# Performance work log

Measured on AMD Instinct MI355X. Metric: run time of the kernel, lower is better.

Reference implementation:

```python
import jax, jax.numpy as jnp
import numpy as np

# Module config (matches init_kwargs shape_data=[8,32,32], pow=1, spde_type='adv_diff')
N_T, N_Y, N_X = 8, 32, 32
N = N_Y * N_X            # nb_nodes
DX = DY = DT = 1.0


def build_A(kappa, m1, m2, h11, h12, h22):
    """Dense [N,N] advection-diffusion operator A = kappa^2 I + m.grad - div(H grad),
    central differences on the n_y x n_x grid, zero-Dirichlet boundary (9-pt stencil).
    All coefficient inputs are [N] vectors (node-wise)."""
    ii, jj = jnp.divmod(jnp.arange(N), N_X)   # ii: y index, jj: x index
    rows = jnp.arange(N)
    A = jnp.zeros((N, N), dtype=kappa.dtype)
    # center
    A = A.at[rows, rows].add(kappa ** 2 + 2.0 * h11 / DX**2 + 2.0 * h22 / DY**2)

    def add(A, di, dj, coef):
        vi, vj = ii + di, jj + dj
        valid = (vi >= 0) & (vi < N_Y) & (vj >= 0) & (vj < N_X)
        cols = jnp.clip(vi, 0, N_Y - 1) * N_X + jnp.clip(vj, 0, N_X - 1)
        return A.at[rows, cols].add(jnp.where(valid, coef, 0.0))

    A = add(A, 0, +1, -h11 / DX**2 + m1 / (2.0 * DX))
    A = add(A, 0, -1, -h11 / DX**2 - m1 / (2.0 * DX))
    A = add(A, +1, 0, -h22 / DY**2 + m2 / (2.0 * DY))
    A = add(A, -1, 0, -h22 / DY**2 - m2 / (2.0 * DY))
    cxy = h12 / (2.0 * DX * DY)    # cross term -2*H12*u_xy with /(4 dx dy) stencil
    A = add(A, +1, +1, -cxy)
    A = add(A, -1, -1, -cxy)
    A = add(A, +1, -1, +cxy)
    A = add(A, -1, +1, +cxy)
    return A


def _forward(kappa, m, H, tau):
    n_b = kappa.shape[0]
    # reorder field params to [n_b, n_t, N]
    kap = jnp.moveaxis(kappa[:, 0], -1, 1)
    m1 = jnp.moveaxis(m[:, 0], -1, 1)
    m2 = jnp.moveaxis(m[:, 1], -1, 1)
    h11 = jnp.moveaxis(H[:, 0, 0], -1, 1)
    h12 = jnp.moveaxis(H[:, 0, 1], -1, 1)
    h22 = jnp.moveaxis(H[:, 1, 1], -1, 1)
    tau_ = jnp.moveaxis(tau[:, 0], -1, 1)

    flat = lambda a: a.reshape(n_b * N_T, N)
    A = jax.vmap(build_A)(flat(kap), flat(m1), flat(m2), flat(h11), flat(h12), flat(h22))
    A = A.reshape(n_b, N_T, N, N)                 # B = A since pow == 1

    eye = jnp.eye(N, dtype=A.dtype)
    M = eye + DT * A                               # inv_M_k = I + dt*B_k, [n_b,n_t,N,N]
    w = DT / (tau_ ** 2)                           # Qs_tilde_k = diag(dt / tau_k^2)

    WM = w[..., :, None] * M                       # diag(w_k) @ M_k
    P = jnp.einsum('btij,btik->btjk', M, WM)       # M_k^T diag(w_k) M_k

    # diagonal blocks: D_k = P_k + diag(w_{k+1}) for k < n_t-1; D_{n_t-1} = P_{n_t-1}
    w_next = jnp.concatenate([w[:, 1:], jnp.zeros_like(w[:, :1])], axis=1)
    D = P + w_next[..., :, None] * eye

    # sub-diagonal block (k, k-1) = -M_k^T diag(w_k), k = 1..n_t-1 (0-block padded at front)
    zblk = jnp.zeros((n_b, 1, N, N), dtype=A.dtype)
    lower = jnp.concatenate([zblk, -jnp.swapaxes(WM[:, 1:], -1, -2)], axis=1)
    # super-diagonal block (k, k+1) = -diag(w_{k+1}) M_{k+1}, k = 0..n_t-2 (0-block at end)
    upper = jnp.concatenate([-WM[:, 1:], zblk], axis=1)

    # block-tridiagonal precision Q, packed as [n_b, 3(diag,lower,upper), n_t, N, N]
    return jnp.stack([D, lower, upper], axis=1)


def setup_inputs() -> dict:
    key = jax.random.key(0)
    ks = jax.random.split(key, 4)
    n_b = 2
    kappa = 0.1 + 0.9 * jax.random.uniform(ks[0], (n_b, 1, N, N_T), dtype=jnp.float32)
    m = 0.2 * jax.random.normal(ks[1], (n_b, 2, N, N_T), dtype=jnp.float32)
    H = jax.random.uniform(ks[2], (n_b, 2, 2, N, N_T), dtype=jnp.float32)
    H = H.at[:, 0, 1].multiply(0.2)
    H = H.at[:, 1, 0].set(H[:, 0, 1])              # symmetric diffusion tensor
    tau = 0.5 + jax.random.uniform(ks[3], (n_b, 1, N, N_T), dtype=jnp.float32)
    return {"kappa": kappa, "m": m, "H": H, "tau": tau}


def reference(kappa, m, H, tau):
    return _forward(kappa, m, H, tau)
```

## Files before the change

kernel.cpp:

```cpp
#include <hip/hip_runtime.h>

#define NT 8
#define NY 32
#define NX 32
#define NN 1024

__device__ __forceinline__ void node_coefs(const float* __restrict__ kap,
                                           const float* __restrict__ m,
                                           const float* __restrict__ H,
                                           const float* __restrict__ tau,
                                           int b, int node, int tc,
                                           int iy, int ix,
                                           float* c , float& w) {
    const int base = node * NT + tc;
    const float kp  = kap[(b * NN) * NT + base];
    const float m1  = m[((b * 2 + 0) * NN) * NT + base];
    const float m2  = m[((b * 2 + 1) * NN) * NT + base];
    const float h11 = H[((b * 4 + 0) * NN) * NT + base];
    const float h12 = H[((b * 4 + 1) * NN) * NT + base];
    const float h22 = H[((b * 4 + 3) * NN) * NT + base];
    const float tv  = tau[(b * NN) * NT + base];
    w = 1.0f / (tv * tv);

    const float cxy = 0.5f * h12;
    const bool ym = iy > 0, yp = iy < NY - 1;
    const bool xm = ix > 0, xp = ix < NX - 1;

    c[4] = 1.0f + kp * kp + 2.0f * h11 + 2.0f * h22;
    c[0] = (ym && xm) ? -cxy               : 0.0f;
    c[1] =  ym        ? (-h22 - 0.5f * m2) : 0.0f;
    c[2] = (ym && xp) ?  cxy               : 0.0f;
    c[3] =  xm        ? (-h11 - 0.5f * m1) : 0.0f;
    c[5] =  xp        ? (-h11 + 0.5f * m1) : 0.0f;
    c[6] = (yp && xm) ?  cxy               : 0.0f;
    c[7] =  yp        ? (-h22 + 0.5f * m2) : 0.0f;
    c[8] = (yp && xp) ? -cxy               : 0.0f;
}

__global__ __launch_bounds__(256) void spde_scatter(const float* __restrict__ kap,
                                                    const float* __restrict__ m,
                                                    const float* __restrict__ H,
                                                    const float* __restrict__ tau,
                                                    float* __restrict__ out) {
    __shared__ float sc[4][9][9];
    __shared__ float sw[4][9];

    const int gb  = blockIdx.x;
    const int j4  = gb & 255;
    const int bt  = gb >> 8;
    const int t   = bt & 7;
    const int b   = bt >> 3;
    const int wid  = threadIdx.x >> 6;
    const int lane = threadIdx.x & 63;
    const int j  = j4 * 4 + wid;
    const int jy = j >> 5, jx = j & 31;

    if (lane < 9) {
        const int ey = lane / 3 - 1, ex = lane % 3 - 1;
        const int iy = jy + ey, ix = jx + ex;
        float c[9];
        float w = 0.0f;
        if (iy >= 0 && iy < NY && ix >= 0 && ix < NX) {
            node_coefs(kap, m, H, tau, b, iy * NX + ix, t, iy, ix, c, w);
        } else {
            #pragma unroll
            for (int q = 0; q < 9; ++q) c[q] = 0.0f;
        }
        #pragma unroll
        for (int q = 0; q < 9; ++q) sc[wid][lane][q] = c[q];
        sw[wid][lane] = w;
    }
    __syncthreads();

    if (lane < 25) {
        const int dy = lane / 5 - 2, dx = lane % 5 - 2;
        const int ky = jy + dy, kx = jx + dx;
        if (ky >= 0 && ky < NY && kx >= 0 && kx < NX) {
            float acc = 0.0f;
            #pragma unroll
            for (int d = 0; d < 9; ++d) {
                const int ey = d / 3 - 1, ex = d % 3 - 1;
                const int r2y = dy - ey, r2x = dx - ex;
                if (r2y >= -1 && r2y <= 1 && r2x >= -1 && r2x <= 1) {
                    acc += sw[wid][d] * sc[wid][d][8 - d]
                }
            }
            if (lane == 12 && t < NT - 1) {
                const float tv = tau[((size_t)b * NN + j) * NT + (t + 1)];
                acc += 1.0f / (tv * tv);
            }
            float* Drow = out + (((size_t)(b * 3 + 0) * NT + t) << 20) + ((size_t)j << 10);
            Drow[ky * NX + kx] = acc;
        }
    } else if (lane >= 32 && lane < 41) {
        if (t > 0) {
            const int d  = lane - 32;
            const int ey = d / 3 - 1, ex = d % 3 - 1;
            const int ky = jy + ey, kx = jx + ex;
            if (ky >= 0 && ky < NY && kx >= 0 && kx < NX) {
                float* Lrow = out + (((size_t)(b * 3 + 1) * NT + t) << 20) + ((size_t)j << 10);
                Lrow[ky * NX + kx] = -sw[wid][d] * sc[wid][d][8 - d];
            }
        }
    } else if (lane >= 48 && lane < 57) {
        if (t > 0) {
            const int q  = lane - 48;
            const int ey = q / 3 - 1, ex = q % 3 - 1;
            const int ky = jy + ey, kx = jx + ex;
            if (ky >= 0 && ky < NY && kx >= 0 && kx < NX) {
                float* Urow = out + (((size_t)(b * 3 + 2) * NT + (t - 1)) << 20) + ((size_t)j << 10);
                Urow[ky * NX + kx] = -sw[wid][4] * sc[wid][4][q];
            }
        }
    }
}

extern "C" void kernel_launch(void* const* d_in, const int* in_sizes, int n_in,
                              void* d_out, int out_size, void* d_ws, size_t ws_size,
                              hipStream_t stream) {
    (void)n_in; (void)d_ws; (void)ws_size;
    const float* kap = (const float*)d_in[0];
    const float* m   = (const float*)d_in[1];
    const float* H   = (const float*)d_in[2];
    const float* tau = (const float*)d_in[3];
    float* out = (float*)d_out;

    const int n_b = in_sizes[0] / (NN * NT);

    hipMemsetAsync(d_out, 0, (size_t)out_size, stream);

    const int grid = n_b * NT * 256;
    spde_scatter<<<grid, 256, 0, stream>>>(kap, m, H, tau, out);
}
```

Measured before the change: 207.0 us.

## Fuse zero-fill with stencil scatter, writing full dense rows via float4 stores

Removes the separate hipMemsetAsync and has the kernel write every element of the D, L and U blocks itself, zeros included, using coalesced float4 stores. Each block now handles 16 consecutive row-nodes and shares a 3x18 halo of node coefficients in LDS, staging the nonzero values before the dense write-out. The aim is to avoid writing the output twice (memset plus scattered stores) and to replace uncoalesced scalar scatter writes with streaming vector writes. For t=0 the kernel writes a zero block into U slot 7, which relies on that slot being all zeros and so overlapping harmlessly with the t=7 case.

```diff
diff --git a/kernel.cpp b/kernel.cpp
--- a/kernel.cpp
+++ b/kernel.cpp
@@ -37,27 +37,28 @@
     c[8] = (yp && xp) ? -cxy               : 0.0f;
 }
 
-__global__ __launch_bounds__(256) void spde_scatter(const float* __restrict__ kap,
-                                                    const float* __restrict__ m,
-                                                    const float* __restrict__ H,
-                                                    const float* __restrict__ tau,
-                                                    float* __restrict__ out) {
-    __shared__ float sc[4][9][9];
-    __shared__ float sw[4][9];
+__global__ __launch_bounds__(256) void spde_fused(const float* __restrict__ kap,
+                                                  const float* __restrict__ m,
+                                                  const float* __restrict__ H,
+                                                  const float* __restrict__ tau,
+                                                  float* __restrict__ out) {
+    __shared__ float sc[3][18][9];
+    __shared__ float sw[3][18];
+    __shared__ float valsD[16][25];
+    __shared__ float valsL[16][9];
+    __shared__ float valsU[16][9];
 
-    const int gb  = blockIdx.x;
-    const int j4  = gb & 255;
-    const int bt  = gb >> 8;
-    const int t   = bt & 7;
-    const int b   = bt >> 3;
-    const int wid  = threadIdx.x >> 6;
-    const int lane = threadIdx.x & 63;
-    const int j  = j4 * 4 + wid;
-    const int jy = j >> 5, jx = j & 31;
+    const int gb   = blockIdx.x;
+    const int half = gb & 1;
+    const int jy   = (gb >> 1) & 31;
+    const int t    = (gb >> 6) & 7;
+    const int b    = gb >> 9;
+    const int jx0  = half * 16;
+    const int tid  = threadIdx.x;
 
-    if (lane < 9) {
-        const int ey = lane / 3 - 1, ex = lane % 3 - 1;
-        const int iy = jy + ey, ix = jx + ex;
+    if (tid < 54) {
+        const int ly = tid / 18, lx = tid % 18;
+        const int iy = jy + ly - 1, ix = jx0 + lx - 1;
         float c[9];
         float w = 0.0f;
         if (iy >= 0 && iy < NY && ix >= 0 && ix < NX) {
@@ -67,58 +68,104 @@
             for (int q = 0; q < 9; ++q) c[q] = 0.0f;
         }
         #pragma unroll
-        for (int q = 0; q < 9; ++q) sc[wid][lane][q] = c[q];
-        sw[wid][lane] = w;
+        for (int q = 0; q < 9; ++q) sc[ly][lx][q] = c[q];
+        sw[ly][lx] = w;
     }
     __syncthreads();
 
-    if (lane < 25) {
-        const int dy = lane / 5 - 2, dx = lane % 5 - 2;
-        const int ky = jy + dy, kx = jx + dx;
-        if (ky >= 0 && ky < NY && kx >= 0 && kx < NX) {
+    #pragma unroll
+    for (int pass = 0; pass < 3; ++pass) {
+        const int e = tid + pass * 256;
+        if (e < 400) {
+            const int jj = e / 25, l = e % 25;
+            const int dy = l / 5 - 2, dx = l % 5 - 2;
             float acc = 0.0f;
             #pragma unroll
             for (int d = 0; d < 9; ++d) {
                 const int ey = d / 3 - 1, ex = d % 3 - 1;
                 const int r2y = dy - ey, r2x = dx - ex;
                 if (r2y >= -1 && r2y <= 1 && r2x >= -1 && r2x <= 1) {
-                    acc += sw[wid][d] * sc[wid][d][8 - d]
+                    const float* ci = sc[ey + 1][jj + 1 + ex];
+                    acc += sw[ey + 1][jj + 1 + ex] * ci[8 - d]
                 }
             }
-            if (lane == 12 && t < NT - 1) {
+            if (l == 12 && t < NT - 1) {
+                const int j = jy * NX + jx0 + jj;
                 const float tv = tau[((size_t)b * NN + j) * NT + (t + 1)];
                 acc += 1.0f / (tv * tv);
             }
-            float* Drow = out + (((size_t)(b * 3 + 0) * NT + t) << 20) + ((size_t)j << 10);
-            Drow[ky * NX + kx] = acc;
+            valsD[jj][l] = acc;
+        } else if (e < 544) {
+            const int e2 = e - 400;
+            const int jj = e2 / 9, d = e2 % 9;
+            const int ey = d / 3 - 1, ex = d % 3 - 1;
+            valsL[jj][d] = -sw[ey + 1][jj + 1 + ex] * sc[ey + 1][jj + 1 + ex][8 - d];
+        } else if (e < 688) {
+            const int e2 = e - 544;
+            const int jj = e2 / 9, qi = e2 % 9;
+            valsU[jj][qi] = -sw[1][jj + 1] * sc[1][jj + 1][qi];
         }
-    } else if (lane >= 32 && lane < 41) {
-        if (t > 0) {
-            const int d  = lane - 32;
-            const int ey = d / 3 - 1, ex = d % 3 - 1;
-            const int ky = jy + ey, kx = jx + ex;
-            if (ky >= 0 && ky < NY && kx >= 0 && kx < NX) {
-                float* Lrow = out + (((size_t)(b * 3 + 1) * NT + t) << 20) + ((size_t)j << 10);
-                Lrow[ky * NX + kx] = -sw[wid][d] * sc[wid][d][8 - d];
+    }
+    __syncthreads();
+
+    const int q   = tid;
+    const int ky  = q >> 3, kx0 = (q & 7) * 4;
+    const int ddy = ky - jy;
+    float4* const outq = (float4*)out;
+    const size_t matD = ((size_t)(b * 3 + 0) * NT + t) << 18;
+    const size_t matL = ((size_t)(b * 3 + 1) * NT + t) << 18;
+    const int ut = (t >= 1) ? (t - 1) : 7;
+    const size_t matU = ((size_t)(b * 3 + 2) * NT + ut) << 18;
+    const bool inD  = (ddy >= -2 && ddy <= 2);
+    const bool inLU = (ddy >= -1 && ddy <= 1);
+
+    #pragma unroll 4
+    for (int jj = 0; jj < 16; ++jj) {
+        const int jx = jx0 + jj;
+        const int j  = jy * NX + jx;
+        const size_t rq = ((size_t)j << 8) + q;
+        float4 vD = make_float4(0.f, 0.f, 0.f, 0.f);
+        float4 vL = make_float4(0.f, 0.f, 0.f, 0.f);
+        float4 vU = make_float4(0.f, 0.f, 0.f, 0.f);
+        if (inD) {
+            float* vp = &vD.x;
+            const float* wrow = &valsD[jj][(ddy + 2) * 5 + 2];
+            #pragma unroll
+            for (int qq = 0; qq < 4; ++qq) {
+                const int ddx = kx0 + qq - jx;
+                if (ddx >= -2 && ddx <= 2) vp[qq] = wrow[ddx];
             }
         }
-    } else if (lane >= 48 && lane < 57) {
-        if (t > 0) {
-            const int q  = lane - 48;
-            const int ey = q / 3 - 1, ex = q % 3 - 1;
-            const int ky = jy + ey, kx = jx + ex;
-            if (ky >= 0 && ky < NY && kx >= 0 && kx < NX) {
-                float* Urow = out + (((size_t)(b * 3 + 2) * NT + (t - 1)) << 20) + ((size_t)j << 10);
-                Urow[ky * NX + kx] = -sw[wid][4] * sc[wid][4][q];
+        if (inLU) {
+            if (t > 0) {
+                float* vp = &vL.x;
+                const float* wrow = &valsL[jj][(ddy + 1) * 3 + 1];
+                #pragma unroll
+                for (int qq = 0; qq < 4; ++qq) {
+                    const int ddx = kx0 + qq - jx;
+                    if (ddx >= -1 && ddx <= 1) vp[qq] = wrow[ddx];
+                }
+            }
+            if (t >= 1) {
+                float* vp = &vU.x;
+                const float* wrow = &valsU[jj][(ddy + 1) * 3 + 1];
+                #pragma unroll
+                for (int qq = 0; qq < 4; ++qq) {
+                    const int ddx = kx0 + qq - jx;
+                    if (ddx >= -1 && ddx <= 1) vp[qq] = wrow[ddx];
+                }
             }
         }
+        outq[matD + rq] = vD;
+        outq[matL + rq] = vL;
+        outq[matU + rq] = vU;
     }
 }
 
 extern "C" void kernel_launch(void* const* d_in, const int* in_sizes, int n_in,
                               void* d_out, int out_size, void* d_ws, size_t ws_size,
                               hipStream_t stream) {
-    (void)n_in; (void)d_ws; (void)ws_size;
+    (void)n_in; (void)d_ws; (void)ws_size; (void)out_size;
     const float* kap = (const float*)d_in[0];
     const float* m   = (const float*)d_in[1];
     const float* H   = (const float*)d_in[2];
@@ -126,9 +173,6 @@
     float* out = (float*)d_out;
 
     const int n_b = in_sizes[0] / (NN * NT);
-
-    hipMemsetAsync(d_out, 0, (size_t)out_size, stream);
-
-    const int grid = n_b * NT * 256;
-    spde_scatter<<<grid, 256, 0, stream>>>(kap, m, H, tau, out);
+    const int grid = n_b * NT * NY * 2;
+    spde_fused<<<grid, 256, 0, stream>>>(kap, m, H, tau, out);
 }
```

After: 201.5 us. 2.6% less time.

## Stage stencil values in shared memory and write output rows as float4 segments

Applied to the files above, without the earlier changes.

Each block now handles 2 rows with 128 threads per row instead of 4 rows with 64, so the grid doubles. Computed D/L/U stencil values go to shared memory first, then each row's nonzero band is written as contiguous float4 stores covering full 32-wide y-rows, padding with zeros. This replaces scattered scalar stores with coalesced vector stores, at the cost of an extra barrier and more threads per row. The memset of the whole output is still done, so the zeros written here are redundant with it.

```diff
diff --git a/kernel.cpp b/kernel.cpp
--- a/kernel.cpp
+++ b/kernel.cpp
@@ -42,21 +42,25 @@
                                                     const float* __restrict__ H,
                                                     const float* __restrict__ tau,
                                                     float* __restrict__ out) {
-    __shared__ float sc[4][9][9];
-    __shared__ float sw[4][9];
+    __shared__ float sc[2][9][9];
+    __shared__ float sw[2][9];
+    __shared__ float valsD[2][25];
+    __shared__ float valsL[2][9];
+    __shared__ float valsU[2][9];
 
-    const int gb  = blockIdx.x;
-    const int j4  = gb & 255;
-    const int bt  = gb >> 8;
-    const int t   = bt & 7;
-    const int b   = bt >> 3;
-    const int wid  = threadIdx.x >> 6;
-    const int lane = threadIdx.x & 63;
-    const int j  = j4 * 4 + wid;
-    const int jy = j >> 5, jx = j & 31;
+    const int gb   = blockIdx.x;
+    const int jp   = gb & 511;
+    const int bt   = gb >> 9;
+    const int t    = bt & 7;
+    const int b    = bt >> 3;
+    const int tid  = threadIdx.x;
+    const int jj   = tid >> 7;
+    const int g    = tid & 127;
+    const int j    = jp * 2 + jj;
+    const int jy   = j >> 5, jx = j & 31;
 
-    if (lane < 9) {
-        const int ey = lane / 3 - 1, ex = lane % 3 - 1;
+    if (g < 9) {
+        const int ey = g / 3 - 1, ex = g % 3 - 1;
         const int iy = jy + ey, ix = jx + ex;
         float c[9];
         float w = 0.0f;
@@ -67,49 +71,74 @@
             for (int q = 0; q < 9; ++q) c[q] = 0.0f;
         }
         #pragma unroll
-        for (int q = 0; q < 9; ++q) sc[wid][lane][q] = c[q];
-        sw[wid][lane] = w;
+        for (int q = 0; q < 9; ++q) sc[jj][g][q] = c[q];
+        sw[jj][g] = w;
     }
     __syncthreads();
 
-    if (lane < 25) {
-        const int dy = lane / 5 - 2, dx = lane % 5 - 2;
-        const int ky = jy + dy, kx = jx + dx;
-        if (ky >= 0 && ky < NY && kx >= 0 && kx < NX) {
-            float acc = 0.0f;
-            #pragma unroll
-            for (int d = 0; d < 9; ++d) {
-                const int ey = d / 3 - 1, ex = d % 3 - 1;
-                const int r2y = dy - ey, r2x = dx - ex;
-                if (r2y >= -1 && r2y <= 1 && r2x >= -1 && r2x <= 1) {
-                    acc += sw[wid][d] * sc[wid][d][8 - d]
-                }
-            }
-            if (lane == 12 && t < NT - 1) {
-                const float tv = tau[((size_t)b * NN + j) * NT + (t + 1)];
-                acc += 1.0f / (tv * tv);
-            }
-            float* Drow = out + (((size_t)(b * 3 + 0) * NT + t) << 20) + ((size_t)j << 10);
-            Drow[ky * NX + kx] = acc;
-        }
-    } else if (lane >= 32 && lane < 41) {
-        if (t > 0) {
-            const int d  = lane - 32;
+    if (g < 25) {
+        const int dy = g / 5 - 2, dx = g % 5 - 2;
+        float acc = 0.0f;
+        #pragma unroll
+        for (int d = 0; d < 9; ++d) {
             const int ey = d / 3 - 1, ex = d % 3 - 1;
-            const int ky = jy + ey, kx = jx + ex;
-            if (ky >= 0 && ky < NY && kx >= 0 && kx < NX) {
-                float* Lrow = out + (((size_t)(b * 3 + 1) * NT + t) << 20) + ((size_t)j << 10);
-                Lrow[ky * NX + kx] = -sw[wid][d] * sc[wid][d][8 - d];
+            const int r2y = dy - ey, r2x = dx - ex;
+            if (r2y >= -1 && r2y <= 1 && r2x >= -1 && r2x <= 1) {
+                acc += sw[jj][d] * sc[jj][d][8 - d]
             }
         }
-    } else if (lane >= 48 && lane < 57) {
-        if (t > 0) {
-            const int q  = lane - 48;
-            const int ey = q / 3 - 1, ex = q % 3 - 1;
-            const int ky = jy + ey, kx = jx + ex;
-            if (ky >= 0 && ky < NY && kx >= 0 && kx < NX) {
-                float* Urow = out + (((size_t)(b * 3 + 2) * NT + (t - 1)) << 20) + ((size_t)j << 10);
-                Urow[ky * NX + kx] = -sw[wid][4] * sc[wid][4][q];
+        if (g == 12 && t < NT - 1) {
+            const float tv = tau[((size_t)b * NN + j) * NT + (t + 1)];
+            acc += 1.0f / (tv * tv);
+        }
+        valsD[jj][g] = acc;
+    } else if (g >= 32 && g < 41) {
+        const int d = g - 32;
+        valsL[jj][d] = -sw[jj][d] * sc[jj][d][8 - d];
+    } else if (g >= 48 && g < 57) {
+        const int q = g - 48;
+        valsU[jj][q] = -sw[jj][4] * sc[jj][4][q];
+    }
+    __syncthreads();
+
+    if (g < 88) {
+        const int s = g >> 3, q = g & 7;
+        float4* const outq = (float4*)out;
+        float4 v = make_float4(0.f, 0.f, 0.f, 0.f);
+        float* vp = &v.x;
+
+        if (s < 5) {
+            const int dy = s - 2, ky = jy + dy;
+            if (ky >= 0 && ky < NY) {
+                #pragma unroll
+                for (int c = 0; c < 4; ++c) {
+                    const int ddx = q * 4 + c - jx;
+                    if (ddx >= -2 && ddx <= 2) vp[c] = valsD[jj][(dy + 2) * 5 + (ddx + 2)];
+                }
+                const size_t matD = ((size_t)(b * 3 + 0) * NT + t) << 18;
+                outq[matD + ((size_t)j << 8) + ky * 8 + q] = v;
+            }
+        } else if (s < 8) {
+            const int dy = s - 6, ky = jy + dy;
+            if (t > 0 && ky >= 0 && ky < NY) {
+                #pragma unroll
+                for (int c = 0; c < 4; ++c) {
+                    const int ddx = q * 4 + c - jx;
+                    if (ddx >= -1 && ddx <= 1) vp[c] = valsL[jj][(dy + 1) * 3 + (ddx + 1)];
+                }
+                const size_t matL = ((size_t)(b * 3 + 1) * NT + t) << 18;
+                outq[matL + ((size_t)j << 8) + ky * 8 + q] = v;
+            }
+        } else {
+            const int dy = s - 9, ky = jy + dy;
+            if (t > 0 && ky >= 0 && ky < NY) {
+                #pragma unroll
+                for (int c = 0; c < 4; ++c) {
+                    const int ddx = q * 4 + c - jx;
+                    if (ddx >= -1 && ddx <= 1) vp[c] = valsU[jj][(dy + 1) * 3 + (ddx + 1)];
+                }
+                const size_t matU = ((size_t)(b * 3 + 2) * NT + (t - 1)) << 18;
+                outq[matU + ((size_t)j << 8) + ky * 8 + q] = v;
             }
         }
     }
@@ -129,6 +158,6 @@
 
     hipMemsetAsync(d_out, 0, (size_t)out_size, stream);
 
-    const int grid = n_b * NT * 256;
+    const int grid = n_b * NT * (NN / 2);
     spde_scatter<<<grid, 256, 0, stream>>>(kap, m, H, tau, out);
 }
```

Result: faster. 194.5 us (-6.0%).

## Fuse zero-fill into chunked dense writer with vectorized full-row stores

Applied to the files above, without the earlier changes.

Drops the separate memset plus sparse scatter and instead has each block own a 64-row chunk of one output matrix. The block computes its stencil values into shared memory and then writes every element of the chunk, zeros included, with coalesced 16-byte stores. This removes the double write of the output (memset, then scatter) and the uncoalesced scattered stores. The cost is more complex indexing, and coefficients are recomputed per chunk for each block type.

```diff
diff --git a/kernel.cpp b/kernel.cpp
--- a/kernel.cpp
+++ b/kernel.cpp
@@ -4,6 +4,8 @@
 #define NY 32
 #define NX 32
 #define NN 1024
+
+typedef __attribute__((ext_vector_type(4))) float f32x4;
 
 __device__ __forceinline__ void node_coefs(const float* __restrict__ kap,
                                            const float* __restrict__ m,
@@ -37,88 +39,136 @@
     c[8] = (yp && xp) ? -cxy               : 0.0f;
 }
 
-__global__ __launch_bounds__(256) void spde_scatter(const float* __restrict__ kap,
-                                                    const float* __restrict__ m,
-                                                    const float* __restrict__ H,
-                                                    const float* __restrict__ tau,
-                                                    float* __restrict__ out) {
-    __shared__ float sc[4][9][9];
-    __shared__ float sw[4][9];
+__global__ __launch_bounds__(256) void spde_chunks(const float* __restrict__ kap,
+                                                   const float* __restrict__ m,
+                                                   const float* __restrict__ H,
+                                                   const float* __restrict__ tau,
+                                                   float* __restrict__ out) {
+    __shared__ float sc[4][34][9];
+    __shared__ float sw[4][34];
+    __shared__ float vals[64][25];
 
-    const int gb  = blockIdx.x;
-    const int j4  = gb & 255;
-    const int bt  = gb >> 8;
-    const int t   = bt & 7;
-    const int b   = bt >> 3;
-    const int wid  = threadIdx.x >> 6;
-    const int lane = threadIdx.x & 63;
-    const int j  = j4 * 4 + wid;
-    const int jy = j >> 5, jx = j & 31;
+    const int chunk = blockIdx.x;
+    const int mat   = chunk >> 4;
+    const int j0    = (chunk & 15) * 64;
+    const int tt    = mat & 7;
+    const int c     = (mat >> 3) % 3;
+    const int b     = mat / 24;
+    const int tid   = threadIdx.x;
+    const int y0    = j0 >> 5;
 
-    if (lane < 9) {
-        const int ey = lane / 3 - 1, ex = lane % 3 - 1;
-        const int iy = jy + ey, ix = jx + ex;
-        float c[9];
+    f32x4* const base = (f32x4*)out + ((size_t)chunk << 14) + tid;
+
+    const bool zeroChunk = (c == 1 && tt == 0) || (c == 2 && tt == NT - 1);
+    if (zeroChunk) {
+        const f32x4 z = {0.f, 0.f, 0.f, 0.f};
+        #pragma unroll
+        for (int k = 0; k < 64; ++k) base[k * 256] = z;
+        return;
+    }
+
+    const int tc = (c == 2) ? tt + 1 : tt;
+
+    if (tid < 136) {
+        const int ly = tid / 34, lx = tid % 34;
+        const int iy = y0 + ly - 1, ix = lx - 1;
+        float cf[9];
         float w = 0.0f;
         if (iy >= 0 && iy < NY && ix >= 0 && ix < NX) {
-            node_coefs(kap, m, H, tau, b, iy * NX + ix, t, iy, ix, c, w);
+            node_coefs(kap, m, H, tau, b, iy * NX + ix, tc, iy, ix, cf, w);
         } else {
             #pragma unroll
-            for (int q = 0; q < 9; ++q) c[q] = 0.0f;
+            for (int q = 0; q < 9; ++q) cf[q] = 0.0f;
         }
         #pragma unroll
-        for (int q = 0; q < 9; ++q) sc[wid][lane][q] = c[q];
-        sw[wid][lane] = w;
+        for (int q = 0; q < 9; ++q) sc[ly][lx][q] = cf[q];
+        sw[ly][lx] = w;
     }
     __syncthreads();
 
-    if (lane < 25) {
-        const int dy = lane / 5 - 2, dx = lane % 5 - 2;
-        const int ky = jy + dy, kx = jx + dx;
-        if (ky >= 0 && ky < NY && kx >= 0 && kx < NX) {
-            float acc = 0.0f;
-            #pragma unroll
-            for (int d = 0; d < 9; ++d) {
-                const int ey = d / 3 - 1, ex = d % 3 - 1;
-                const int r2y = dy - ey, r2x = dx - ex;
-                if (r2y >= -1 && r2y <= 1 && r2x >= -1 && r2x <= 1) {
-                    acc += sw[wid][d] * sc[wid][d][8 - d]
+    if (c == 0) {
+        #pragma unroll
+        for (int pass = 0; pass < 7; ++pass) {
+            const int e = tid + pass * 256;
+            if (e < 1600) {
+                const int k = e / 25, l = e % 25;
+                const int dy = l / 5 - 2, dx = l % 5 - 2;
+                const int ry = k >> 5, jx = k & 31;
+                float acc = 0.0f;
+                #pragma unroll
+                for (int d = 0; d < 9; ++d) {
+                    const int ey = d / 3 - 1, ex = d % 3 - 1;
+                    const int r2y = dy - ey, r2x = dx - ex;
+                    if (r2y >= -1 && r2y <= 1 && r2x >= -1 && r2x <= 1) {
+                        const float* ci = sc[ry + 1 + ey][jx + 1 + ex];
+                        acc += sw[ry + 1 + ey][jx + 1 + ex] * ci[8 - d]
+                    }
                 }
-            }
-            if (lane == 12 && t < NT - 1) {
-                const float tv = tau[((size_t)b * NN + j) * NT + (t + 1)];
-                acc += 1.0f / (tv * tv);
-            }
-            float* Drow = out + (((size_t)(b * 3 + 0) * NT + t) << 20) + ((size_t)j << 10);
-            Drow[ky * NX + kx] = acc;
-        }
-    } else if (lane >= 32 && lane < 41) {
-        if (t > 0) {
-            const int d  = lane - 32;
-            const int ey = d / 3 - 1, ex = d % 3 - 1;
-            const int ky = jy + ey, kx = jx + ex;
-            if (ky >= 0 && ky < NY && kx >= 0 && kx < NX) {
-                float* Lrow = out + (((size_t)(b * 3 + 1) * NT + t) << 20) + ((size_t)j << 10);
-                Lrow[ky * NX + kx] = -sw[wid][d] * sc[wid][d][8 - d];
+                if (l == 12 && tt < NT - 1) {
+                    const int j = j0 + k;
+                    const float tv = tau[((size_t)b * NN + j) * NT + (tt + 1)];
+                    acc += 1.0f / (tv * tv);
+                }
+                vals[k][l] = acc;
             }
         }
-    } else if (lane >= 48 && lane < 57) {
-        if (t > 0) {
-            const int q  = lane - 48;
-            const int ey = q / 3 - 1, ex = q % 3 - 1;
-            const int ky = jy + ey, kx = jx + ex;
-            if (ky >= 0 && ky < NY && kx >= 0 && kx < NX) {
-                float* Urow = out + (((size_t)(b * 3 + 2) * NT + (t - 1)) << 20) + ((size_t)j << 10);
-                Urow[ky * NX + kx] = -sw[wid][4] * sc[wid][4][q];
+    } else if (c == 1) {
+        #pragma unroll
+        for (int pass = 0; pass < 3; ++pass) {
+            const int e = tid + pass * 256;
+            if (e < 576) {
+                const int k = e / 9, d = e % 9;
+                const int ey = d / 3 - 1, ex = d % 3 - 1;
+                const int ly = (k >> 5) + 1 + ey, lx = (k & 31) + 1 + ex;
+                vals[k][d] = -sw[ly][lx] * sc[ly][lx][8 - d];
             }
         }
+    } else {
+        #pragma unroll
+        for (int pass = 0; pass < 3; ++pass) {
+            const int e = tid + pass * 256;
+            if (e < 576) {
+                const int k = e / 9, q = e % 9;
+                const int ly = (k >> 5) + 1, lx = (k & 31) + 1;
+                vals[k][q] = -sw[ly][lx] * sc[ly][lx][q];
+            }
+        }
+    }
+    __syncthreads();
+
+    const int ky  = tid >> 3, kx0 = (tid & 7) * 4;
+    const int R   = (c == 0) ? 2 : 1;
+    const int nw  = 2 * R + 1;
+    f32x4* p = base;
+    #pragma unroll
+    for (int h = 0; h < 2; ++h) {
+        const int jy  = y0 + h;
+        const int ddy = ky - jy;
+        if (ddy < -R || ddy > R) {
+            const f32x4 z = {0.f, 0.f, 0.f, 0.f};
+            #pragma unroll
+            for (int kk = 0; kk < 32; ++kk) p[kk * 256] = z;
+        } else {
+            const int rowoff = (ddy + R) * nw + R;
+            #pragma unroll
+            for (int kk = 0; kk < 32; ++kk) {
+                f32x4 v = {0.f, 0.f, 0.f, 0.f};
+                #pragma unroll
+                for (int cq = 0; cq < 4; ++cq) {
+                    const int ddx = kx0 + cq - kk;
+                    if (ddx >= -R && ddx <= R) v[cq] = vals[h * 32 + kk][rowoff + ddx];
+                }
+                p[kk * 256] = v;
+            }
+        }
+        p += 32 * 256;
     }
 }
 
 extern "C" void kernel_launch(void* const* d_in, const int* in_sizes, int n_in,
                               void* d_out, int out_size, void* d_ws, size_t ws_size,
                               hipStream_t stream) {
-    (void)n_in; (void)d_ws; (void)ws_size;
+    (void)n_in; (void)d_ws; (void)ws_size; (void)out_size;
     const float* kap = (const float*)d_in[0];
     const float* m   = (const float*)d_in[1];
     const float* H   = (const float*)d_in[2];
@@ -126,9 +176,6 @@
     float* out = (float*)d_out;
 
     const int n_b = in_sizes[0] / (NN * NT);
-
-    hipMemsetAsync(d_out, 0, (size_t)out_size, stream);
-
-    const int grid = n_b * NT * 256;
-    spde_scatter<<<grid, 256, 0, stream>>>(kap, m, H, tau, out);
+    const int grid = n_b * 3 * NT * 16;
+    spde_chunks<<<grid, 256, 0, stream>>>(kap, m, H, tau, out);
 }
```

New measurement: 202.8 us. -2.0%, faster.
